# Performance work log

Measured on AMD Instinct MI355X. Metric: run time of the kernel, lower is better.

The kernel has to match this reference:

```python
import jax, jax.numpy as jnp
import numpy as np

DIM = 1024


def setup_inputs() -> dict:
    key = jax.random.key(0)
    kx, kw = jax.random.split(key)
    x = jax.random.normal(kx, (4, 2048, DIM), dtype=jnp.float32)
    # fused qkv projection weight, torch Linear convention: [out_features, in_features]
    W_qkv = jax.random.normal(kw, (3 * DIM, DIM), dtype=jnp.float32) * (DIM ** -0.5)
    return {"x": x, "W_qkv": W_qkv}


def reference(x, W_qkv):
    # fused QKV projection: y = x @ W^T -> [B, N, 3*DIM]
    qkv = jnp.einsum('bnd,ed->bne', x, W_qkv)
    B, N, _ = qkv.shape
    # rearrange 'b n (e d) -> e b n d' with e=3
    qkv = qkv.reshape(B, N, 3, DIM).transpose(2, 0, 1, 3)
    q, k, v = qkv[0], qkv[1], qkv[2]
    scale = DIM ** (-0.5)  # note: scale uses full dim, module never splits heads
    attn = jnp.einsum('bnd,bmd->bnm', q * scale, k)  # [B, N, N]
    attn = jax.nn.softmax(attn, axis=-1)
    out = jnp.einsum('bnm,bmd->bnd', attn, v)
    return out
```

## Files before the change

kernel.cpp:

```cpp
#include <hip/hip_runtime.h>

using half8   = __attribute__((ext_vector_type(8))) _Float16;
using f32x4   = __attribute__((ext_vector_type(4))) float;
using ushort8 = __attribute__((ext_vector_type(8))) unsigned short;

__device__ __forceinline__ void gload16(const void* g, void* l) {
  __builtin_amdgcn_global_load_lds(
      (const __attribute__((address_space(1))) void*)g,
      (__attribute__((address_space(3))) void*)l, 16, 0, 0);
}

__device__ __forceinline__ void xcd_swizzle(int& x, int& y, int& z) {
  const int gx = gridDim.x, gy = gridDim.y;
  const int nwg = gx * gy * gridDim.z;
  const int f = blockIdx.x + gx * (blockIdx.y + gy * blockIdx.z);
  const int w = (f & 7) * (nwg >> 3) + (f >> 3);
  const int r = w >> 5, u = w & 31;
  const int nrx = gx >> 3, nry = gy >> 2;
  const int pz  = nrx * nry;
  const int rz  = r / pz, rr = r % pz;
  x = (rr % nrx) * 8 + (u & 7);
  y = (rr / nrx) * 4 + (u >> 3);
  z = rz;
}

__global__ __launch_bounds__(256) void cast_f32_f16(
    const float* __restrict__ in, unsigned short* __restrict__ out, long n) {
  long i = ((long)blockIdx.x * 256 + threadIdx.x) * 8;
  if (i >= n) return;
  float4 a = *(const float4*)(in + i);
  float4 b = *(const float4*)(in + i + 4);
  union { _Float16 h[8]; ushort8 u; } r;
  r.h[0] = (_Float16)a.x; r.h[1] = (_Float16)a.y;
  r.h[2] = (_Float16)a.z; r.h[3] = (_Float16)a.w;
  r.h[4] = (_Float16)b.x; r.h[5] = (_Float16)b.y;
  r.h[6] = (_Float16)b.z; r.h[7] = (_Float16)b.w;
  *(ushort8*)(out + i) = r.u;
}

#define FENCE_N()                                                                  \
  do {                                                                             \
    if constexpr (N_REP == 2)      asm volatile("s_waitcnt vmcnt(2)" ::: "memory");\
    else                           asm volatile("s_waitcnt vmcnt(3)" ::: "memory");\
  } while (0)

#define WAIT_B()                                                                   \
  do {                                                                             \
    if constexpr (N_REP == 2)      asm volatile("s_waitcnt lgkmcnt(4)" ::: "memory");\
    else                           asm volatile("s_waitcnt lgkmcnt(6)" ::: "memory");\
  } while (0)

#define PHASE(P, AF, BC, BNX)                                                      \
  {                                                                                \
    _Pragma("unroll") for (int i = 0; i < 2; ++i) {                                \
      AF[i][0] = *(const half8*)(lA + aRd + (2 * (P) + i) * 2048 + kg0);           \
      AF[i][1] = *(const half8*)(lA + aRd + (2 * (P) + i) * 2048 + kg1);           \
    }                                                                              \
    if ((P) == 3) {            \
      _Pragma("unroll") for (int ni = 0; ni < N_REP; ++ni) {                       \
        BNX[ni][0] = *(const half8*)(lBn + bRd + ni * 2048 + kg0);                 \
        BNX[ni][1] = *(const half8*)(lBn + bRd + ni * 2048 + kg1);                 \
      }                                                                            \
    }                                                                              \
    __builtin_amdgcn_sched_barrier(0);                                             \
    __builtin_amdgcn_s_barrier();                                                  \
    if ((P) == 3) WAIT_B();                                                        \
    else asm volatile("s_waitcnt lgkmcnt(0)" ::: "memory");                        \
    __builtin_amdgcn_sched_barrier(0);                                             \
    if ((P) == 0 && t + 1 < nt) {                          \
      unsigned short* d = ldsA + (SLOT ^ 1) * ASZ + wv * 512;                      \
      const long kt = (long)(t + 1) * 64;                                          \
      gload16(aS + kt, d);                                                         \
      gload16(aS + (long)64 * lda + kt, d + 4096);                                 \
      gload16(aS + (long)128 * lda + kt, d + 8192);                                \
      gload16(aS + (long)192 * lda + kt, d + 12288);                               \
    }                                                                              \
    if ((P) == 1 && t + 2 < nt) {   \
      const long kt = (long)(t + 2) * 64;                                          \
      _Pragma("unroll") for (int j = 0; j < N_REP; ++j)                            \
        gload16(bS + (long)(j * 64) * ldb + kt,                                    \
                ldsB + SLOT * BSZ + j * 4096 + wv * 512);                          \
    }                                                                              \
    __builtin_amdgcn_s_setprio(1);                                                 \
    _Pragma("unroll") for (int ks = 0; ks < 2; ++ks)                               \
    _Pragma("unroll") for (int i = 0; i < 2; ++i)                                  \
    _Pragma("unroll") for (int ni = 0; ni < N_REP; ++ni)                           \
      acc[2 * (P) + i][ni] = __builtin_amdgcn_mfma_f32_16x16x32_f16(               \
          AF[i][ks], BC[ni][ks], acc[2 * (P) + i][ni], 0, 0, 0);                   \
    __builtin_amdgcn_s_setprio(0);                                                 \
    __builtin_amdgcn_sched_barrier(0);                                             \
    if ((P) == 2) {                                                                \
      if (t + 2 < nt) FENCE_N();                                                   \
      else asm volatile("s_waitcnt vmcnt(0)" ::: "memory");                        \
      __builtin_amdgcn_s_barrier();                                                \
    }                                                                              \
  }

#define TILE(T, S, BC, BNX)                                                        \
  {                                                                                \
    const int t = (T);                                                             \
    constexpr int SLOT = (S);                                                      \
    const char* lA  = (const char*)(ldsA + SLOT * ASZ);                            \
    const char* lBn = (const char*)(ldsB + (SLOT ^ 1) * BSZ);                      \
    PHASE(0, afA, BC, BNX)                                                         \
    PHASE(1, afB, BC, BNX)                                                         \
    PHASE(2, afA, BC, BNX)                                                         \
    PHASE(3, afB, BC, BNX)                                                         \
  }

template <int MODE, int N_REP>
__global__ __launch_bounds__(512, 2) void gemm8p(
    const unsigned short* __restrict__ Ab, const unsigned short* __restrict__ Bb,
    int K, int lda, int ldb, long sA, long sB,
    void* __restrict__ o0, void* __restrict__ o1, void* __restrict__ o2) {
  constexpr int BM  = 256;
  constexpr int BN  = 64 * N_REP;
  constexpr int ASZ = BM * 64;
  constexpr int BSZ = BN * 64;
  __shared__ unsigned short lds[2 * ASZ + 2 * BSZ];

  const int tid  = threadIdx.x;
  const int lane = tid & 63;
  const int wv   = tid >> 6;
  const int wr   = wv >> 2, wc = wv & 3;
  const int fr   = lane & 15, fq = lane >> 4;
  int bxi, byi, bzi;
  xcd_swizzle(bxi, byi, bzi);
  const int bm = byi * BM;
  const int bn = bxi * BN;
  const int bz = bzi;

  const unsigned short* A = Ab + (long)bz * sA;
  const unsigned short* B = Bb + (long)bz * sB;

  const int row_s = tid >> 3;
  const int col_s = ((tid & 7) ^ (row_s & 7)) * 8;
  const unsigned short* aS = A + (long)(bm + row_s) * lda + col_s;
  const unsigned short* bS = B + (long)(bn + row_s) * ldb + col_s;
  unsigned short* ldsA = lds;
  unsigned short* ldsB = lds + 2 * ASZ;

  const int kg0 = ((0 * 4 + fq) ^ (fr & 7)) * 16;
  const int kg1 = ((1 * 4 + fq) ^ (fr & 7)) * 16;
  const int aRd = (wr * 128 + fr) * 128;
  const int bRd = (wc * (16 * N_REP) + fr) * 128;

  f32x4 acc[8][N_REP] = {};
  half8 afA[2][2], afB[2][2];
  half8 bf0[N_REP][2], bf1[N_REP][2];

  const int nt = K / 64;

#pragma unroll
  for (int i = 0; i < 4; ++i)
    gload16(aS + (long)(i * 64) * lda, ldsA + i * 4096 + wv * 512);
#pragma unroll
  for (int j = 0; j < N_REP; ++j)
    gload16(bS + (long)(j * 64) * ldb, ldsB + j * 4096 + wv * 512);
#pragma unroll
  for (int j = 0; j < N_REP; ++j)
    gload16(bS + (long)(j * 64) * ldb + 64, ldsB + BSZ + j * 4096 + wv * 512);
  FENCE_N();
  __builtin_amdgcn_s_barrier();
  {
    const char* lB0 = (const char*)ldsB;
#pragma unroll
    for (int ni = 0; ni < N_REP; ++ni) {
      bf0[ni][0] = *(const half8*)(lB0 + bRd + ni * 2048 + kg0);
      bf0[ni][1] = *(const half8*)(lB0 + bRd + ni * 2048 + kg1);
    }
  }

  for (int tt = 0; tt < nt; tt += 2) {
    TILE(tt, 0, bf0, bf1)
    TILE(tt + 1, 1, bf1, bf0)
  }

  const int row0 = bm + wr * 128 + fq * 4;
  const int col0 = bn + wc * (16 * N_REP) + fr;
#pragma unroll
  for (int mi = 0; mi < 8; ++mi) {
#pragma unroll
    for (int ni = 0; ni < N_REP; ++ni) {
      f32x4 c = acc[mi][ni];
      const long r0 = row0 + mi * 16;
      const long e  = col0 + ni * 16;
      if constexpr (MODE == 0) {
        _Float16* q  = (_Float16*)o0;
        _Float16* kk = (_Float16*)o1;
        _Float16* vv = (_Float16*)o2;
#pragma unroll
        for (int j = 0; j < 4; ++j) {
          const long i = r0 + j;
          const float val = c[j];
          if (e < 1024)      q [i * 1024 + e]          = (_Float16)(val * 0.03125f);
          else if (e < 2048) kk[i * 1024 + (e - 1024)] = (_Float16)val;
          else               vv[i * 1024 + (e - 2048)] = (_Float16)val;
        }
      } else if constexpr (MODE == 1) {
        float* C = (float*)o0 + (long)bz * 2048 * 2048;
#pragma unroll
        for (int j = 0; j < 4; ++j) C[(r0 + j) * 2048 + e] = c[j];
      } else {
        float* C = (float*)o0 + (long)bz * 2048 * 1024;
#pragma unroll
        for (int j = 0; j < 4; ++j) C[(r0 + j) * 1024 + e] = c[j];
      }
    }
  }
}

__global__ __launch_bounds__(256) void transpose_v(
    const unsigned short* __restrict__ v, unsigned short* __restrict__ vT) {
  __shared__ unsigned short t[64][72];
  const long b = blockIdx.z;
  const unsigned short* vb = v + b * (2048L * 1024);
  unsigned short* ob = vT + b * (1024L * 2048);
  const int n0 = blockIdx.y * 64;
  const int d0 = blockIdx.x * 64;
  const int tid = threadIdx.x;
  const int r  = tid >> 2;
  const int c0 = (tid & 3) * 16;
  const unsigned short* src = vb + (long)(n0 + r) * 1024 + d0 + c0;
  *(ushort4*)&t[r][c0]      = *(const ushort4*)(src);
  *(ushort4*)&t[r][c0 + 4]  = *(const ushort4*)(src + 4);
  *(ushort4*)&t[r][c0 + 8]  = *(const ushort4*)(src + 8);
  *(ushort4*)&t[r][c0 + 12] = *(const ushort4*)(src + 12);
  __syncthreads();
  union { unsigned short h[8]; ushort8 u; } w0, w1;
#pragma unroll
  for (int j = 0; j < 8; ++j) w0.h[j] = t[c0 + j][r];
#pragma unroll
  for (int j = 0; j < 8; ++j) w1.h[j] = t[c0 + 8 + j][r];
  unsigned short* dst = ob + (long)(d0 + r) * 2048 + n0 + c0;
  *(ushort8*)dst       = w0.u;
  *(ushort8*)(dst + 8) = w1.u;
}

__global__ __launch_bounds__(256) void softmax_rows(float* __restrict__ S) {
  const long row = blockIdx.x;
  float* p = S + row * 2048;
  const int t = threadIdx.x;
  float4 v0 = *(const float4*)(p + t * 8);
  float4 v1 = *(const float4*)(p + t * 8 + 4);
  float f[8] = {v0.x, v0.y, v0.z, v0.w, v1.x, v1.y, v1.z, v1.w};
  float m = f[0];
#pragma unroll
  for (int j = 1; j < 8; ++j) m = fmaxf(m, f[j]);
  for (int o = 32; o; o >>= 1) m = fmaxf(m, __shfl_xor(m, o));
  __shared__ float redm[4];
  if (!(t & 63)) redm[t >> 6] = m;
  __syncthreads();
  m = fmaxf(fmaxf(redm[0], redm[1]), fmaxf(redm[2], redm[3]));
  float e[8], s = 0.f;
#pragma unroll
  for (int j = 0; j < 8; ++j) { e[j] = __expf(f[j] - m); s += e[j]; }
  for (int o = 32; o; o >>= 1) s += __shfl_xor(s, o);
  __shared__ float reds[4];
  if (!(t & 63)) reds[t >> 6] = s;
  __syncthreads();
  s = reds[0] + reds[1] + reds[2] + reds[3];
  const float inv = 1.0f / s;
  union { _Float16 h[8]; ushort8 u; } r;
#pragma unroll
  for (int j = 0; j < 8; ++j) r.h[j] = (_Float16)(e[j] * inv);
  *(ushort8*)((unsigned short*)p + t * 8) = r.u;
}

extern "C" void kernel_launch(void* const* d_in, const int* in_sizes, int n_in,
                              void* d_out, int out_size, void* d_ws, size_t ws_size,
                              hipStream_t stream) {
  const float* x = (const float*)d_in[0];
  const float* W = (const float*)d_in[1];
  float* out = (float*)d_out;
  char* ws = (char*)d_ws;

  const long MB16 = 16777216;
  unsigned short* q  = (unsigned short*)(ws);
  unsigned short* k  = (unsigned short*)(ws + MB16);
  unsigned short* vT = (unsigned short*)(ws + 2 * MB16);
  float*          S  = (float*)(ws + 3 * MB16);
  unsigned short* xb = (unsigned short*)(ws + 3 * MB16);
  unsigned short* wb = (unsigned short*)(ws + 4 * MB16);
  unsigned short* v  = (unsigned short*)(ws + 4 * MB16 + 6291456);

  cast_f32_f16<<<4096, 256, 0, stream>>>(x, xb, 8388608L);
  cast_f32_f16<<<1536, 256, 0, stream>>>(W, wb, 3145728L);
  gemm8p<0, 3><<<dim3(16, 32, 1), 512, 0, stream>>>(
      xb, wb, 1024, 1024, 1024, 0L, 0L, q, k, v);
  transpose_v<<<dim3(16, 32, 4), 256, 0, stream>>>(v, vT);
  gemm8p<1, 2><<<dim3(16, 8, 4), 512, 0, stream>>>(
      q, k, 1024, 1024, 1024, 2048L * 1024, 2048L * 1024, S, nullptr, nullptr);
  softmax_rows<<<8192, 256, 0, stream>>>(S);
  gemm8p<2, 2><<<dim3(8, 8, 4), 512, 0, stream>>>(
      (unsigned short*)S, vT, 2048, 4096, 2048, 2048L * 4096, 1024L * 2048,
      out, nullptr, nullptr);
}
```

Measured before the change: 175.3 us.

## Restructure GEMM pipeline into 8 phases with finer-grained staged prefetch

Replaces the 4-phase tile pipeline with an 8-phase loop that issues global->LDS loads for A and B in smaller chunks spread across phases, loads B fragments once per tile, and interleaves warp rows (stride 16 instead of contiguous 128-row blocks). The QK^T GEMM is switched to a 256x256 tile (N_REP=4) with half the grid in x. The aim is to spread memory traffic more evenly across compute phases and raise data reuse per block. In exchange it adds a barrier every phase and larger per-block register use, which may lower occupancy or cause stalls.

```diff
diff --git a/kernel.cpp b/kernel.cpp
--- a/kernel.cpp
+++ b/kernel.cpp
@@ -38,76 +38,6 @@
   *(ushort8*)(out + i) = r.u;
 }
 
-#define FENCE_N()                                                                  \
-  do {                                                                             \
-    if constexpr (N_REP == 2)      asm volatile("s_waitcnt vmcnt(2)" ::: "memory");\
-    else                           asm volatile("s_waitcnt vmcnt(3)" ::: "memory");\
-  } while (0)
-
-#define WAIT_B()                                                                   \
-  do {                                                                             \
-    if constexpr (N_REP == 2)      asm volatile("s_waitcnt lgkmcnt(4)" ::: "memory");\
-    else                           asm volatile("s_waitcnt lgkmcnt(6)" ::: "memory");\
-  } while (0)
-
-#define PHASE(P, AF, BC, BNX)                                                      \
-  {                                                                                \
-    _Pragma("unroll") for (int i = 0; i < 2; ++i) {                                \
-      AF[i][0] = *(const half8*)(lA + aRd + (2 * (P) + i) * 2048 + kg0);           \
-      AF[i][1] = *(const half8*)(lA + aRd + (2 * (P) + i) * 2048 + kg1);           \
-    }                                                                              \
-    if ((P) == 3) {            \
-      _Pragma("unroll") for (int ni = 0; ni < N_REP; ++ni) {                       \
-        BNX[ni][0] = *(const half8*)(lBn + bRd + ni * 2048 + kg0);                 \
-        BNX[ni][1] = *(const half8*)(lBn + bRd + ni * 2048 + kg1);                 \
-      }                                                                            \
-    }                                                                              \
-    __builtin_amdgcn_sched_barrier(0);                                             \
-    __builtin_amdgcn_s_barrier();                                                  \
-    if ((P) == 3) WAIT_B();                                                        \
-    else asm volatile("s_waitcnt lgkmcnt(0)" ::: "memory");                        \
-    __builtin_amdgcn_sched_barrier(0);                                             \
-    if ((P) == 0 && t + 1 < nt) {                          \
-      unsigned short* d = ldsA + (SLOT ^ 1) * ASZ + wv * 512;                      \
-      const long kt = (long)(t + 1) * 64;                                          \
-      gload16(aS + kt, d);                                                         \
-      gload16(aS + (long)64 * lda + kt, d + 4096);                                 \
-      gload16(aS + (long)128 * lda + kt, d + 8192);                                \
-      gload16(aS + (long)192 * lda + kt, d + 12288);                               \
-    }                                                                              \
-    if ((P) == 1 && t + 2 < nt) {   \
-      const long kt = (long)(t + 2) * 64;                                          \
-      _Pragma("unroll") for (int j = 0; j < N_REP; ++j)                            \
-        gload16(bS + (long)(j * 64) * ldb + kt,                                    \
-                ldsB + SLOT * BSZ + j * 4096 + wv * 512);                          \
-    }                                                                              \
-    __builtin_amdgcn_s_setprio(1);                                                 \
-    _Pragma("unroll") for (int ks = 0; ks < 2; ++ks)                               \
-    _Pragma("unroll") for (int i = 0; i < 2; ++i)                                  \
-    _Pragma("unroll") for (int ni = 0; ni < N_REP; ++ni)                           \
-      acc[2 * (P) + i][ni] = __builtin_amdgcn_mfma_f32_16x16x32_f16(               \
-          AF[i][ks], BC[ni][ks], acc[2 * (P) + i][ni], 0, 0, 0);                   \
-    __builtin_amdgcn_s_setprio(0);                                                 \
-    __builtin_amdgcn_sched_barrier(0);                                             \
-    if ((P) == 2) {                                                                \
-      if (t + 2 < nt) FENCE_N();                                                   \
-      else asm volatile("s_waitcnt vmcnt(0)" ::: "memory");                        \
-      __builtin_amdgcn_s_barrier();                                                \
-    }                                                                              \
-  }
-
-#define TILE(T, S, BC, BNX)                                                        \
-  {                                                                                \
-    const int t = (T);                                                             \
-    constexpr int SLOT = (S);                                                      \
-    const char* lA  = (const char*)(ldsA + SLOT * ASZ);                            \
-    const char* lBn = (const char*)(ldsB + (SLOT ^ 1) * BSZ);                      \
-    PHASE(0, afA, BC, BNX)                                                         \
-    PHASE(1, afB, BC, BNX)                                                         \
-    PHASE(2, afA, BC, BNX)                                                         \
-    PHASE(3, afB, BC, BNX)                                                         \
-  }
-
 template <int MODE, int N_REP>
 __global__ __launch_bounds__(512, 2) void gemm8p(
     const unsigned short* __restrict__ Ab, const unsigned short* __restrict__ Bb,
@@ -142,48 +72,114 @@
 
   const int kg0 = ((0 * 4 + fq) ^ (fr & 7)) * 16;
   const int kg1 = ((1 * 4 + fq) ^ (fr & 7)) * 16;
-  const int aRd = (wr * 128 + fr) * 128;
+  const int aRd = (wr * 16 + fr) * 128;
   const int bRd = (wc * (16 * N_REP) + fr) * 128;
 
   f32x4 acc[8][N_REP] = {};
-  half8 afA[2][2], afB[2][2];
-  half8 bf0[N_REP][2], bf1[N_REP][2];
+  half8 bf[N_REP][2];
+  half8 afX[2][2], afY[2][2];
 
   const int nt = K / 64;
 
-#pragma unroll
-  for (int i = 0; i < 4; ++i)
-    gload16(aS + (long)(i * 64) * lda, ldsA + i * 4096 + wv * 512);
-#pragma unroll
-  for (int j = 0; j < N_REP; ++j)
-    gload16(bS + (long)(j * 64) * ldb, ldsB + j * 4096 + wv * 512);
-#pragma unroll
-  for (int j = 0; j < N_REP; ++j)
-    gload16(bS + (long)(j * 64) * ldb + 64, ldsB + BSZ + j * 4096 + wv * 512);
-  FENCE_N();
+#define FENCE_K1()                                                                 \
+  do {                                                                             \
+    if constexpr (N_REP == 2)      asm volatile("s_waitcnt vmcnt(4)" ::: "memory");\
+    else if constexpr (N_REP == 3) asm volatile("s_waitcnt vmcnt(5)" ::: "memory");\
+    else                           asm volatile("s_waitcnt vmcnt(6)" ::: "memory");\
+  } while (0)
+#define VM0() asm volatile("s_waitcnt vmcnt(0)" ::: "memory")
+
+#define STAGE_A01(SL, T) {                                                         \
+    const long kt = (long)(T) * 64;                                                \
+    unsigned short* d = ldsA + (SL) * ASZ + wv * 512;                              \
+    gload16(aS + kt, d);                                                           \
+    gload16(aS + (long)64 * lda + kt, d + 4096); }
+#define STAGE_A23(SL, T) {                                                         \
+    const long kt = (long)(T) * 64;                                                \
+    unsigned short* d = ldsA + (SL) * ASZ + 8192 + wv * 512;                       \
+    gload16(aS + (long)128 * lda + kt, d);                                         \
+    gload16(aS + (long)192 * lda + kt, d + 4096); }
+#define STAGE_B0(SL, T) {                                                          \
+    const long kt = (long)(T) * 64;                                                \
+    unsigned short* d = ldsB + (SL) * BSZ + wv * 512;                              \
+    gload16(bS + kt, d);                                                           \
+    gload16(bS + (long)64 * ldb + kt, d + 4096); }
+#define STAGE_B1(SL, T)                                                            \
+    if constexpr (N_REP >= 3) {                                                    \
+      const long kt = (long)(T) * 64;                                              \
+      unsigned short* d = ldsB + (SL) * BSZ + 8192 + wv * 512;                     \
+      gload16(bS + (long)128 * ldb + kt, d);                                       \
+      if constexpr (N_REP == 4) gload16(bS + (long)192 * ldb + kt, d + 4096);      \
+    }
+
+#define PH(P, AF)                                                                  \
+  {                                                                                \
+    constexpr int SL = ((P) >= 4) ? 1 : 0;                                         \
+    const char* lA = (const char*)(ldsA + SL * ASZ);                               \
+    if ((P) == 0 || (P) == 4) {                                                    \
+      const char* lB = (const char*)(ldsB + SL * BSZ);                             \
+      _Pragma("unroll") for (int ni = 0; ni < N_REP; ++ni) {                       \
+        bf[ni][0] = *(const half8*)(lB + bRd + ni * 2048 + kg0);                   \
+        bf[ni][1] = *(const half8*)(lB + bRd + ni * 2048 + kg1);                   \
+      }                                                                            \
+    }                                                                              \
+    _Pragma("unroll") for (int i = 0; i < 2; ++i) {                                \
+      AF[i][0] = *(const half8*)(lA + aRd + (2 * ((P) & 3) + i) * 4096 + kg0);     \
+      AF[i][1] = *(const half8*)(lA + aRd + (2 * ((P) & 3) + i) * 4096 + kg1);     \
+    }                                                                              \
+    if ((P) == 0)               STAGE_A23(1, t + 1)                                \
+    if ((P) == 1 && t + 2 < nt) STAGE_B0(0, t + 2)                                 \
+    if ((P) == 2 && t + 2 < nt) STAGE_A01(0, t + 2)                                \
+    if ((P) == 3 && t + 2 < nt) STAGE_B1(0, t + 2)                                 \
+    if ((P) == 4 && t + 2 < nt) STAGE_A23(0, t + 2)                                \
+    if ((P) == 5 && t + 3 < nt) STAGE_B0(1, t + 3)                                 \
+    if ((P) == 6 && t + 3 < nt) STAGE_A01(1, t + 3)                                \
+    if ((P) == 7 && t + 3 < nt) STAGE_B1(1, t + 3)                                 \
+    __builtin_amdgcn_sched_barrier(0);                                             \
+    __builtin_amdgcn_s_barrier();                                                  \
+    asm volatile("s_waitcnt lgkmcnt(0)" ::: "memory");                             \
+    __builtin_amdgcn_sched_barrier(0);                                             \
+    __builtin_amdgcn_s_setprio(1);                                                 \
+    _Pragma("unroll") for (int ks = 0; ks < 2; ++ks)                               \
+    _Pragma("unroll") for (int i = 0; i < 2; ++i)                                  \
+    _Pragma("unroll") for (int ni = 0; ni < N_REP; ++ni)                           \
+      acc[2 * ((P) & 3) + i][ni] = __builtin_amdgcn_mfma_f32_16x16x32_f16(         \
+          AF[i][ks], bf[ni][ks], acc[2 * ((P) & 3) + i][ni], 0, 0, 0);             \
+    __builtin_amdgcn_s_setprio(0);                                                 \
+    __builtin_amdgcn_sched_barrier(0);                                             \
+    if ((P) == 3) { if (t + 2 < nt) FENCE_K1(); else VM0(); }                      \
+    if ((P) == 7) { if (t + 3 < nt) FENCE_K1(); else VM0(); }                      \
+    __builtin_amdgcn_s_barrier();                                                  \
+  }
+
+  STAGE_A01(0, 0)
+  STAGE_A23(0, 0)
+  STAGE_B0(0, 0)
+  STAGE_B1(0, 0)
+  STAGE_A01(1, 1)
+  STAGE_B0(1, 1)
+  STAGE_B1(1, 1)
+  FENCE_K1();
   __builtin_amdgcn_s_barrier();
-  {
-    const char* lB0 = (const char*)ldsB;
-#pragma unroll
-    for (int ni = 0; ni < N_REP; ++ni) {
-      bf0[ni][0] = *(const half8*)(lB0 + bRd + ni * 2048 + kg0);
-      bf0[ni][1] = *(const half8*)(lB0 + bRd + ni * 2048 + kg1);
-    }
+
+  for (int t = 0; t < nt; t += 2) {
+    PH(0, afX) PH(1, afY) PH(2, afX) PH(3, afY)
+    PH(4, afX) PH(5, afY) PH(6, afX) PH(7, afY)
   }
-
-  for (int tt = 0; tt < nt; tt += 2) {
-    TILE(tt, 0, bf0, bf1)
-    TILE(tt + 1, 1, bf1, bf0)
-  }
-
-  const int row0 = bm + wr * 128 + fq * 4;
+#undef PH
+#undef STAGE_A01
+#undef STAGE_A23
+#undef STAGE_B0
+#undef STAGE_B1
+
+  const int row0 = bm + wr * 16 + fq * 4;
   const int col0 = bn + wc * (16 * N_REP) + fr;
 #pragma unroll
   for (int mi = 0; mi < 8; ++mi) {
 #pragma unroll
     for (int ni = 0; ni < N_REP; ++ni) {
       f32x4 c = acc[mi][ni];
-      const long r0 = row0 + mi * 16;
+      const long r0 = row0 + mi * 32;
       const long e  = col0 + ni * 16;
       if constexpr (MODE == 0) {
         _Float16* q  = (_Float16*)o0;
@@ -289,7 +285,7 @@
   gemm8p<0, 3><<<dim3(16, 32, 1), 512, 0, stream>>>(
       xb, wb, 1024, 1024, 1024, 0L, 0L, q, k, v);
   transpose_v<<<dim3(16, 32, 4), 256, 0, stream>>>(v, vT);
-  gemm8p<1, 2><<<dim3(16, 8, 4), 512, 0, stream>>>(
+  gemm8p<1, 4><<<dim3(8, 8, 4), 512, 0, stream>>>(
       q, k, 1024, 1024, 1024, 2048L * 1024, 2048L * 1024, S, nullptr, nullptr);
   softmax_rows<<<8192, 256, 0, stream>>>(S);
   gemm8p<2, 2><<<dim3(8, 8, 4), 512, 0, stream>>>(
```

After: 176.3 us. No clear change (+0.6%).
